# Performance work log

Measured on AMD Instinct MI355X. Metric: run time of the kernel, lower is better.

The kernel has to match this reference:

```python
import jax, jax.numpy as jnp
import numpy as np

EPS = 1e-5  # equinox LayerNorm default eps

def setup_inputs() -> dict:
    key = jax.random.key(0)
    k1, k2, k3, k4, k5 = jax.random.split(key, 5)
    heads, d, dH, N = 16, 1024, 64, 2048
    # lecun-normal-ish scaling for fan_in=d
    s = 1.0 / np.sqrt(d)
    return {
        "x": jax.random.normal(k1, (d, N), dtype=jnp.float32),
        "WQ": jax.random.normal(k2, (heads, d, dH), dtype=jnp.float32) * s,
        "WK": jax.random.normal(k3, (heads, d, dH), dtype=jnp.float32) * s,
        "WV": jax.random.normal(k4, (heads, d, dH), dtype=jnp.float32) * s,
        "W0": jax.random.normal(k5, (d, d), dtype=jnp.float32) * s,
    }

def reference(x, WQ, WK, WV, W0):
    # x: [d, N]
    residual = x
    # equinox LayerNorm over full shape (d, N), no affine params
    mean = jnp.mean(x)
    var = jnp.var(x)
    xn = (x - mean) * jax.lax.rsqrt(var + EPS)
    # project: [h, d_model, dH] x [d_model, N] -> [h, dH, N]
    Q = jnp.einsum('hcd,ci->hdi', WQ, xn)
    K = jnp.einsum('hcd,ci->hdi', WK, xn)
    V = jnp.einsum('hcd,ci->hdi', WV, xn)
    dH = WK.shape[-1]
    dot = jnp.einsum('hdi,hdj->hij', Q, K)  # [h, N, N]
    alpha = jax.nn.softmax(dot / jnp.sqrt(jnp.asarray(dH, dot.dtype)), axis=-1)
    attn = jnp.einsum('hij,hdj->hdi', alpha, V)  # [h, dH, N]
    N = attn.shape[2]
    attn = attn.reshape(-1, N)  # [d, N]
    out = W0 @ attn
    return out + residual
```

## Files before the change

### kernel.cpp

```cpp
#include <hip/hip_runtime.h>
#include <math.h>

typedef unsigned short u16;
typedef _Float16 f16;
typedef __attribute__((ext_vector_type(8))) short bf16x8;
typedef __attribute__((ext_vector_type(4))) float f32x4;
typedef __attribute__((ext_vector_type(4))) f16 f16x4;

#define D_MODEL 1024
#define SEQ_N   2048
#define HEADS   16
#define DHEAD   64
#define M3      3072
#define JSPLIT  2
#define JCHUNK  (SEQ_N / JSPLIT)
#define NIT     (JCHUNK / 64)
#define QSCALE  0.18033688011112042f
#define EXPOFF  5.770780163555854f

#define GLOBAL_AS __attribute__((address_space(1)))
#define LDS_AS    __attribute__((address_space(3)))
#define ASYNC16(gp, lp) __builtin_amdgcn_global_load_lds( \
    (const GLOBAL_AS unsigned int*)(gp), (LDS_AS unsigned int*)(lp), 16, 0, 0)

__device__ __forceinline__ u16 f2bf(float f) {
  union { float f; unsigned int u; } v; v.f = f;
  unsigned int r = v.u + 0x7fffu + ((v.u >> 16) & 1u);
  return (u16)(r >> 16);
}

__global__ __launch_bounds__(256) void prep(const float* __restrict__ x,
                                            double* __restrict__ part,
                                            const float* __restrict__ WQ,
                                            const float* __restrict__ WK,
                                            const float* __restrict__ WV,
                                            const float* __restrict__ W0,
                                            u16* __restrict__ Wp,
                                            u16* __restrict__ W0p) {
  __shared__ double ls[256], lss[256];
  __shared__ float tile[32][65];
  int t = threadIdx.x;
  int b = blockIdx.x;
  if (b < 256) {
    const float4* x4 = (const float4*)x;
    const int n4 = (D_MODEL * SEQ_N) / 4;
    double s = 0.0, ss = 0.0;
    for (int idx = b * 256 + t; idx < n4; idx += 256 * 256) {
      float4 v = x4[idx];
      s  += (double)v.x + (double)v.y + (double)v.z + (double)v.w;
      ss += (double)v.x * v.x + (double)v.y * v.y + (double)v.z * v.z + (double)v.w * v.w;
    }
    ls[t] = s; lss[t] = ss;
    __syncthreads();
    for (int off = 128; off > 0; off >>= 1) {
      if (t < off) { ls[t] += ls[t + off]; lss[t] += lss[t + off]; }
      __syncthreads();
    }
    if (t == 0) { part[2 * b] = ls[0]; part[2 * b + 1] = lss[0]; }
    return;
  }
  int f = b - 256;
  int z = f >> 9;
  int rem = f & 511;
  if (z == 3) {
    int idx = rem * 512 + t;
#pragma unroll
    for (int r = 0; r < 2; ++r, idx += 256) {
      float4 v = ((const float4*)W0)[idx];
      unsigned int lo = (unsigned int)f2bf(v.x) | ((unsigned int)f2bf(v.y) << 16);
      unsigned int hi = (unsigned int)f2bf(v.z) | ((unsigned int)f2bf(v.w) << 16);
      uint2 o; o.x = lo; o.y = hi;
      *(uint2*)(&W0p[(size_t)idx * 4]) = o;
    }
    return;
  }
  const float* W = (z == 0) ? WQ : ((z == 1) ? WK : WV);
  int h = rem >> 5, cb = (rem & 31) * 32;
  int dh = t & 63, cl = t >> 6;
  for (int r = 0; r < 8; ++r) {
    int c = cl + r * 4;
    tile[c][dh] = W[((size_t)h * D_MODEL + cb + c) * DHEAD + dh];
  }
  __syncthreads();
  int c2 = t & 31, d2 = t >> 5;
  for (int r = 0; r < 8; ++r) {
    int dd = d2 + r * 8;
    Wp[(size_t)((z * HEADS + h) * DHEAD + dd) * D_MODEL + cb + c2] = f2bf(tile[c2][dd]);
  }
}

__global__ __launch_bounds__(256) void ln_norm_t(const float* __restrict__ x,
                                                 const double* __restrict__ part,
                                                 u16* __restrict__ xnt) {
  __shared__ double ls[256], lss[256];
  __shared__ float tile[64][65];
  int t = threadIdx.x;
  ls[t] = part[2 * t]; lss[t] = part[2 * t + 1];
  __syncthreads();
  for (int off = 128; off > 0; off >>= 1) {
    if (t < off) { ls[t] += ls[t + off]; lss[t] += lss[t + off]; }
    __syncthreads();
  }
  double inv = 1.0 / ((double)D_MODEL * (double)SEQ_N);
  double m = ls[0] * inv;
  double vv = lss[0] * inv - m * m;
  float mean = (float)m;
  float rstd = (float)(1.0 / sqrt(vv + 1e-5));

  int ib = blockIdx.x * 64, cb = blockIdx.y * 64;
  int il = t & 63, cl = t >> 6;
  for (int r = 0; r < 16; ++r) {
    int c = cl + r * 4;
    tile[c][il] = (x[(size_t)(cb + c) * SEQ_N + ib + il] - mean) * rstd;
  }
  __syncthreads();
  int c2 = t & 63, i2 = t >> 6;
  for (int r = 0; r < 16; ++r) {
    int i = i2 + r * 4;
    xnt[(size_t)(ib + i) * D_MODEL + cb + c2] = f2bf(tile[c2][i]);
  }
}

__global__ __launch_bounds__(256) void gemm_qkv(const u16* __restrict__ A,
                                                const u16* __restrict__ Bt,
                                                u16* __restrict__ Qt,
                                                u16* __restrict__ Kt,
                                                f16* __restrict__ Vb) {
  __shared__ __align__(16) u16 Alds[2 * 2 * 96 * 32];
  __shared__ __align__(16) u16 Blds[2 * 2 * 128 * 32];
  int t = threadIdx.x;
  int lane = t & 63, w = t >> 6;
  int g = lane >> 4, l16 = lane & 15;
  int wr = w >> 1, wc = w & 1;
  int flat = blockIdx.x;
  int wi = flat >> 3;
  int wx = wi & 7, wy = wi >> 3;
  int cx = (flat & 7) & 1, cy = (flat & 7) >> 1;
  int bx = cx * 8 + wx;
  int by = cy * 8 + wy;
  int mb = by * 96, nb = bx * 128;

  f32x4 acc[3][4];
#pragma unroll
  for (int i = 0; i < 3; ++i)
#pragma unroll
    for (int j = 0; j < 4; ++j) acc[i][j] = (f32x4){0.f, 0.f, 0.f, 0.f};

  const u16* AgP[3]; int ldsA[3];
#pragma unroll
  for (int r = 0; r < 3; ++r) {
    int idx = r * 256 + t;
    int kk = (idx >= 384) ? 1 : 0;
    int rem = idx - kk * 384;
    int row = rem >> 2, c4 = rem & 3;
    int csw = c4 ^ ((row >> 1) & 3);
    AgP[r] = A + (size_t)(mb + row) * D_MODEL + kk * 32 + csw * 8;
    ldsA[r] = idx * 8;
  }
  const u16* BgP[4]; int ldsB[4];
#pragma unroll
  for (int r = 0; r < 4; ++r) {
    int idx = r * 256 + t;
    int kk = idx >> 9;
    int rem = idx & 511;
    int row = rem >> 2, c4 = rem & 3;
    int csw = c4 ^ ((row >> 1) & 3);
    BgP[r] = Bt + (size_t)(nb + row) * D_MODEL + kk * 32 + csw * 8;
    ldsB[r] = idx * 8;
  }

#pragma unroll
  for (int r = 0; r < 3; ++r) ASYNC16(AgP[r], &Alds[ldsA[r]]);
#pragma unroll
  for (int r = 0; r < 4; ++r) ASYNC16(BgP[r], &Blds[ldsB[r]]);
#pragma unroll
  for (int r = 0; r < 3; ++r) ASYNC16(AgP[r] + 64, &Alds[6144 + ldsA[r]]);
#pragma unroll
  for (int r = 0; r < 4; ++r) ASYNC16(BgP[r] + 64, &Blds[8192 + ldsB[r]]);

  int rowa0 = wr * 48, rowb0 = wc * 64;
  int cur = 0;
  for (int ks = 0; ks < 16; ++ks) {
    if (ks < 15) asm volatile("s_waitcnt vmcnt(7)" ::: "memory");
    else         asm volatile("s_waitcnt vmcnt(0)" ::: "memory");
    __builtin_amdgcn_s_barrier();
#pragma unroll
    for (int kk = 0; kk < 2; ++kk) {
      bf16x8 af[3], bf[4];
#pragma unroll
      for (int tm = 0; tm < 3; ++tm) {
        int row = rowa0 + tm * 16 + l16;
        int gs = g ^ ((row >> 1) & 3);
        af[tm] = *(const bf16x8*)(&Alds[cur * 6144 + kk * 3072 + row * 32 + gs * 8]);
      }
#pragma unroll
      for (int tn = 0; tn < 4; ++tn) {
        int row = rowb0 + tn * 16 + l16;
        int gs = g ^ ((row >> 1) & 3);
        bf[tn] = *(const bf16x8*)(&Blds[cur * 8192 + kk * 4096 + row * 32 + gs * 8]);
      }
#pragma unroll
      for (int tm = 0; tm < 3; ++tm)
#pragma unroll
        for (int tn = 0; tn < 4; ++tn)
          acc[tm][tn] = __builtin_amdgcn_mfma_f32_16x16x32_bf16(af[tm], bf[tn],
                                                                acc[tm][tn], 0, 0, 0);
    }
    __builtin_amdgcn_s_barrier();
    if (ks + 2 < 16) {
      int kb = (ks + 2) * 64;
#pragma unroll
      for (int r = 0; r < 3; ++r) ASYNC16(AgP[r] + kb, &Alds[cur * 6144 + ldsA[r]]);
#pragma unroll
      for (int r = 0; r < 4; ++r) ASYNC16(BgP[r] + kb, &Blds[cur * 8192 + ldsB[r]]);
    }
    cur ^= 1;
  }

#pragma unroll
  for (int tm = 0; tm < 3; ++tm) {
    int row0 = mb + wr * 48 + tm * 16 + g * 4;
#pragma unroll
    for (int tn = 0; tn < 4; ++tn) {
      int col = nb + wc * 64 + tn * 16 + l16;
      if (row0 < 2 * D_MODEL) {
        u16* T = (row0 < D_MODEL) ? Qt : Kt;
        float sc = (row0 < D_MODEL) ? QSCALE : 1.0f;
        int rbase = (row0 < D_MODEL) ? row0 : row0 - D_MODEL;
        ushort4 o;
        o.x = f2bf(acc[tm][tn][0] * sc); o.y = f2bf(acc[tm][tn][1] * sc);
        o.z = f2bf(acc[tm][tn][2] * sc); o.w = f2bf(acc[tm][tn][3] * sc);
        *(ushort4*)(&T[(size_t)col * D_MODEL + rbase]) = o;
      } else {
        int rbase = row0 - 2 * D_MODEL;
#pragma unroll
        for (int r = 0; r < 4; ++r)
          Vb[(size_t)(rbase + r) * SEQ_N + col] = (f16)acc[tm][tn][r];
      }
    }
  }
}

__global__ __launch_bounds__(256) void gemm_bf16(const u16* __restrict__ A,
                                                 const u16* __restrict__ Bt,
                                                 float* __restrict__ C,
                                                 const float* __restrict__ res,
                                                 int M, int N, int K) {
  __shared__ __align__(16) u16 Alds[2 * 2 * 64 * 32];
  __shared__ __align__(16) u16 Blds[2 * 2 * 64 * 32];
  int t = threadIdx.x;
  int w = t >> 6, lane = t & 63;
  int g = lane >> 4, l16 = lane & 15;
  int flat = blockIdx.x;
  int wi = flat >> 3;
  int wx = wi & 7, wy = wi >> 3;
  int cx = (flat & 7) & 3, cy = (flat & 7) >> 2;
  int bx = cx * 8 + wx;
  int by = cy * 8 + wy;
  int mb = by * 64, nb = bx * 64;
  f32x4 acc[4];
  for (int i = 0; i < 4; ++i) acc[i] = (f32x4){0.f, 0.f, 0.f, 0.f};

  const u16* AgP[2]; const u16* BgP[2]; int ldsO[2];
#pragma unroll
  for (int r = 0; r < 2; ++r) {
    int idx = r * 256 + t;
    int kk = idx >> 8;
    int rem = idx & 255;
    int row = rem >> 2, c4 = rem & 3;
    int csw = c4 ^ ((row >> 1) & 3);
    AgP[r] = A + (size_t)(mb + row) * K + kk * 32 + csw * 8;
    BgP[r] = Bt + (size_t)(nb + row) * K + kk * 32 + csw * 8;
    ldsO[r] = idx * 8;
  }

#pragma unroll
  for (int r = 0; r < 2; ++r) { ASYNC16(AgP[r], &Alds[ldsO[r]]); ASYNC16(BgP[r], &Blds[ldsO[r]]); }
#pragma unroll
  for (int r = 0; r < 2; ++r) {
    ASYNC16(AgP[r] + 64, &Alds[4096 + ldsO[r]]);
    ASYNC16(BgP[r] + 64, &Blds[4096 + ldsO[r]]);
  }

  int cur = 0;
  const int NK = 16;
  for (int ks = 0; ks < NK; ++ks) {
    if (ks < NK - 1) asm volatile("s_waitcnt vmcnt(4)" ::: "memory");
    else             asm volatile("s_waitcnt vmcnt(0)" ::: "memory");
    __builtin_amdgcn_s_barrier();
#pragma unroll
    for (int kk = 0; kk < 2; ++kk) {
      int rowa = w * 16 + l16;
      int gsa = g ^ ((rowa >> 1) & 3);
      bf16x8 af = *(const bf16x8*)(&Alds[cur * 4096 + kk * 2048 + rowa * 32 + gsa * 8]);
#pragma unroll
      for (int tn = 0; tn < 4; ++tn) {
        int rowb = tn * 16 + l16;
        int gsb = g ^ ((rowb >> 1) & 3);
        bf16x8 bf = *(const bf16x8*)(&Blds[cur * 4096 + kk * 2048 + rowb * 32 + gsb * 8]);
        acc[tn] = __builtin_amdgcn_mfma_f32_16x16x32_bf16(af, bf, acc[tn], 0, 0, 0);
      }
    }
    __builtin_amdgcn_s_barrier();
    if (ks + 2 < NK) {
      int kb = (ks + 2) * 64;
#pragma unroll
      for (int r = 0; r < 2; ++r) {
        ASYNC16(AgP[r] + kb, &Alds[cur * 4096 + ldsO[r]]);
        ASYNC16(BgP[r] + kb, &Blds[cur * 4096 + ldsO[r]]);
      }
    }
    cur ^= 1;
  }
  int col0 = nb + l16;
  int row0 = mb + w * 16 + g * 4;
#pragma unroll
  for (int tn = 0; tn < 4; ++tn) {
    int col = col0 + tn * 16;
#pragma unroll
    for (int r = 0; r < 4; ++r) {
      int row = row0 + r;
      float v = acc[tn][r];
      if (res) v += res[(size_t)row * N + col];
      C[(size_t)row * N + col] = v;
    }
  }
}

#define KSW(buf_, row_, ch_) ((buf_)*4096 + (row_)*64 + ((((ch_) ^ ((row_)&7)))*8))
__global__ __launch_bounds__(256, 2) void attn_mfma(const u16* __restrict__ Qt,
                                                    const u16* __restrict__ Kt,
                                                    const f16* __restrict__ Vb,
                                                    f16* __restrict__ Opart,
                                                    float* __restrict__ Lpart) {
  __shared__ __align__(16) u16 Klds[2 * 64 * 64];
  __shared__ __align__(16) f16 Vlds[2 * 64 * 64];
  int flat = blockIdx.x;
  int xcd = flat & 7, idx = flat >> 3;
  int h  = xcd * 2 + ((idx >> 5) & 1);
  int sp = idx >> 6;
  int ib = (idx & 31) * 64;
  int j0 = sp * JCHUNK;
  int t = threadIdx.x;
  int w = t >> 6, lane = t & 63;
  int g = lane >> 4, l16 = lane & 15;

  bf16x8 bq[2];
  {
    const u16* qb = Qt + (size_t)(ib + w * 16 + l16) * D_MODEL + h * DHEAD + g * 8;
    bq[0] = *(const bf16x8*)(qb);
    bq[1] = *(const bf16x8*)(qb + 32);
  }

  f32x4 acc_o[4];
#pragma unroll
  for (int i = 0; i < 4; ++i) acc_o[i] = (f32x4){0.f, 0.f, 0.f, 0.f};
  f32x4 acc_l = (f32x4){0.f, 0.f, 0.f, 0.f};
  f16x4 ones;
  ones[0] = (f16)1.f; ones[1] = (f16)1.f; ones[2] = (f16)1.f; ones[3] = (f16)1.f;

  const u16* KgP[2]; const f16* VgP[2]; int ldsS[2];
#pragma unroll
  for (int r = 0; r < 2; ++r) {
    int s = r * 256 + t;
    int row = s >> 3, pch = s & 7;
    int lch = pch ^ (row & 7);
    KgP[r] = Kt + (size_t)(j0 + row) * D_MODEL + h * DHEAD + lch * 8;
    VgP[r] = Vb + (size_t)(h * DHEAD + row) * SEQ_N + j0 + lch * 8;
    ldsS[r] = s * 8;
  }

#pragma unroll
  for (int r = 0; r < 2; ++r) { ASYNC16(KgP[r], &Klds[ldsS[r]]); ASYNC16(VgP[r], &Vlds[ldsS[r]]); }
#pragma unroll
  for (int r = 0; r < 2; ++r) {
    ASYNC16(KgP[r] + 64 * D_MODEL, &Klds[4096 + ldsS[r]]);
    ASYNC16(VgP[r] + 64,           &Vlds[4096 + ldsS[r]]);
  }

  int cur = 0;
  for (int it = 0; it < NIT; ++it) {
    if (it < NIT - 1) asm volatile("s_waitcnt vmcnt(4)" ::: "memory");
    else              asm volatile("s_waitcnt vmcnt(0)" ::: "memory");
    __builtin_amdgcn_s_barrier();

    f32x4 s[4];
#pragma unroll
    for (int i = 0; i < 4; ++i) s[i] = (f32x4){0.f, 0.f, 0.f, 0.f};
    __builtin_amdgcn_s_setprio(1);
#pragma unroll
    for (int kk = 0; kk < 2; ++kk)
#pragma unroll
      for (int tn = 0; tn < 4; ++tn) {
        int row = tn * 16 + l16;
        bf16x8 ak = *(const bf16x8*)(&Klds[KSW(cur, row, kk * 4 + g)]);
        s[tn] = __builtin_amdgcn_mfma_f32_16x16x32_bf16(ak, bq[kk], s[tn], 0, 0, 0);
      }
    __builtin_amdgcn_s_setprio(0);
    f16x4 pf[4];
#pragma unroll
    for (int tn = 0; tn < 4; ++tn) {
      f16x4 p;
#pragma unroll
      for (int r = 0; r < 4; ++r)
        p[r] = (f16)exp2f(s[tn][r] - EXPOFF);
      pf[tn] = p;
    }
    __builtin_amdgcn_s_setprio(1);
#pragma unroll
    for (int tn = 0; tn < 4; ++tn) {
      acc_l = __builtin_amdgcn_mfma_f32_16x16x16f16(pf[tn], ones, acc_l, 0, 0, 0);
#pragma unroll
      for (int td = 0; td < 4; ++td) {
        int row = td * 16 + l16;
        f16x4 bv = *(const f16x4*)(&Vlds[KSW(cur, row, tn * 2 + (g >> 1)) + (g & 1) * 4]);
        acc_o[td] =
            __builtin_amdgcn_mfma_f32_16x16x16f16(pf[tn], bv, acc_o[td], 0, 0, 0);
      }
    }
    __builtin_amdgcn_s_setprio(0);

    __builtin_amdgcn_s_barrier();
    if (it + 2 < NIT) {
      int joff = (it + 2) * 64;
#pragma unroll
      for (int r = 0; r < 2; ++r) {
        ASYNC16(KgP[r] + (size_t)joff * D_MODEL, &Klds[cur * 4096 + ldsS[r]]);
        ASYNC16(VgP[r] + joff,                   &Vlds[cur * 4096 + ldsS[r]]);
      }
    }
    cur ^= 1;
  }

  if (l16 == 0) {
#pragma unroll
    for (int r = 0; r < 4; ++r)
      Lpart[((size_t)sp * HEADS + h) * SEQ_N + ib + w * 16 + g * 4 + r] = acc_l[r];
  }

#pragma unroll
  for (int td = 0; td < 4; ++td) {
    int dh = h * DHEAD + td * 16 + l16;
#pragma unroll
    for (int r = 0; r < 4; ++r) {
      int i = ib + w * 16 + g * 4 + r;
      Opart[((size_t)sp * SEQ_N + i) * D_MODEL + dh] = (f16)acc_o[td][r];
    }
  }
}

__global__ __launch_bounds__(256) void attn_combine(const f16* __restrict__ Opart,
                                                    const float* __restrict__ Lpart,
                                                    u16* __restrict__ attnt) {
  int i = blockIdx.x;
  int c = threadIdx.x * 4;
  int h = c >> 6;
  float l = 0.f;
#pragma unroll
  for (int s = 0; s < JSPLIT; ++s) l += Lpart[((size_t)s * HEADS + h) * SEQ_N + i];
  float o[4] = {0.f, 0.f, 0.f, 0.f};
#pragma unroll
  for (int s = 0; s < JSPLIT; ++s) {
    f16x4 v = *(const f16x4*)(&Opart[((size_t)s * SEQ_N + i) * D_MODEL + c]);
#pragma unroll
    for (int r = 0; r < 4; ++r) o[r] += (float)v[r];
  }
  float inv = 1.0f / l;
  ushort4 ob;
  ob.x = f2bf(o[0] * inv); ob.y = f2bf(o[1] * inv);
  ob.z = f2bf(o[2] * inv); ob.w = f2bf(o[3] * inv);
  *(ushort4*)(&attnt[(size_t)i * D_MODEL + c]) = ob;
}

extern "C" void kernel_launch(void* const* d_in, const int* in_sizes, int n_in,
                              void* d_out, int out_size, void* d_ws, size_t ws_size,
                              hipStream_t stream) {
  const float* x  = (const float*)d_in[0];
  const float* WQ = (const float*)d_in[1];
  const float* WK = (const float*)d_in[2];
  const float* WV = (const float*)d_in[3];
  const float* W0 = (const float*)d_in[4];
  float* out = (float*)d_out;

  char* ws = (char*)d_ws;
  size_t off = 0;
  double* part  = (double*)(ws + off); off += 8192;
  u16*    xnt   = (u16*)(ws + off); off += (size_t)SEQ_N * D_MODEL * 2;
  u16*    Wp    = (u16*)(ws + off); off += (size_t)M3 * D_MODEL * 2;
  u16*    W0p   = (u16*)(ws + off); off += (size_t)D_MODEL * D_MODEL * 2;
  u16*    Qt    = (u16*)(ws + off); off += (size_t)SEQ_N * D_MODEL * 2;
  u16*    Kt    = (u16*)(ws + off); off += (size_t)SEQ_N * D_MODEL * 2;
  f16*    Vb    = (f16*)(ws + off); off += (size_t)D_MODEL * SEQ_N * 2;
  u16*    attnt = (u16*)(ws + off); off += (size_t)SEQ_N * D_MODEL * 2;
  f16*    Opart = (f16*)(ws + off); off += (size_t)JSPLIT * SEQ_N * D_MODEL * 2;
  float*  Lpart = (float*)(ws + off); off += (size_t)JSPLIT * HEADS * SEQ_N * 4;

  prep<<<256 + 2048, 256, 0, stream>>>(x, part, WQ, WK, WV, W0, Wp, W0p);
  ln_norm_t<<<dim3(SEQ_N / 64, D_MODEL / 64), 256, 0, stream>>>(x, part, xnt);
  gemm_qkv<<<512, 256, 0, stream>>>(Wp, xnt, Qt, Kt, Vb);
  attn_mfma<<<1024, 256, 0, stream>>>(Qt, Kt, Vb, Opart, Lpart);
  attn_combine<<<SEQ_N, 256, 0, stream>>>(Opart, Lpart, attnt);
  gemm_bf16<<<512, 256, 0, stream>>>(W0p, attnt, out, x, D_MODEL, SEQ_N, D_MODEL);
}
```

Before: 151.5 us.

## Double query rows per attention block to reuse K/V tiles across two M-subtiles

```diff
diff --git a/kernel.cpp b/kernel.cpp
--- a/kernel.cpp
+++ b/kernel.cpp
@@ -337,25 +337,30 @@
   __shared__ __align__(16) f16 Vlds[2 * 64 * 64];
   int flat = blockIdx.x;
   int xcd = flat & 7, idx = flat >> 3;
-  int h  = xcd * 2 + ((idx >> 5) & 1);
-  int sp = idx >> 6;
-  int ib = (idx & 31) * 64;
+  int h  = xcd * 2 + ((idx >> 4) & 1);
+  int sp = idx >> 5;
+  int ib = (idx & 15) * 128;
   int j0 = sp * JCHUNK;
   int t = threadIdx.x;
   int w = t >> 6, lane = t & 63;
   int g = lane >> 4, l16 = lane & 15;
 
-  bf16x8 bq[2];
-  {
-    const u16* qb = Qt + (size_t)(ib + w * 16 + l16) * D_MODEL + h * DHEAD + g * 8;
-    bq[0] = *(const bf16x8*)(qb);
-    bq[1] = *(const bf16x8*)(qb + 32);
-  }
-
-  f32x4 acc_o[4];
-#pragma unroll
-  for (int i = 0; i < 4; ++i) acc_o[i] = (f32x4){0.f, 0.f, 0.f, 0.f};
-  f32x4 acc_l = (f32x4){0.f, 0.f, 0.f, 0.f};
+  bf16x8 bq[2][2];
+#pragma unroll
+  for (int tm = 0; tm < 2; ++tm) {
+    const u16* qb = Qt + (size_t)(ib + w * 32 + tm * 16 + l16) * D_MODEL + h * DHEAD + g * 8;
+    bq[tm][0] = *(const bf16x8*)(qb);
+    bq[tm][1] = *(const bf16x8*)(qb + 32);
+  }
+
+  f32x4 acc_o[2][4];
+#pragma unroll
+  for (int tm = 0; tm < 2; ++tm)
+#pragma unroll
+    for (int i = 0; i < 4; ++i) acc_o[tm][i] = (f32x4){0.f, 0.f, 0.f, 0.f};
+  f32x4 acc_l[2];
+  acc_l[0] = (f32x4){0.f, 0.f, 0.f, 0.f};
+  acc_l[1] = (f32x4){0.f, 0.f, 0.f, 0.f};
   f16x4 ones;
   ones[0] = (f16)1.f; ones[1] = (f16)1.f; ones[2] = (f16)1.f; ones[3] = (f16)1.f;
 
@@ -384,9 +389,11 @@
     else              asm volatile("s_waitcnt vmcnt(0)" ::: "memory");
     __builtin_amdgcn_s_barrier();
 
-    f32x4 s[4];
-#pragma unroll
-    for (int i = 0; i < 4; ++i) s[i] = (f32x4){0.f, 0.f, 0.f, 0.f};
+    f32x4 s[2][4];
+#pragma unroll
+    for (int tm = 0; tm < 2; ++tm)
+#pragma unroll
+      for (int i = 0; i < 4; ++i) s[tm][i] = (f32x4){0.f, 0.f, 0.f, 0.f};
     __builtin_amdgcn_s_setprio(1);
 #pragma unroll
     for (int kk = 0; kk < 2; ++kk)
@@ -394,28 +401,36 @@
       for (int tn = 0; tn < 4; ++tn) {
         int row = tn * 16 + l16;
         bf16x8 ak = *(const bf16x8*)(&Klds[KSW(cur, row, kk * 4 + g)]);
-        s[tn] = __builtin_amdgcn_mfma_f32_16x16x32_bf16(ak, bq[kk], s[tn], 0, 0, 0);
+#pragma unroll
+        for (int tm = 0; tm < 2; ++tm)
+          s[tm][tn] = __builtin_amdgcn_mfma_f32_16x16x32_bf16(ak, bq[tm][kk],
+                                                              s[tm][tn], 0, 0, 0);
       }
     __builtin_amdgcn_s_setprio(0);
-    f16x4 pf[4];
+    f16x4 pf[2][4];
+#pragma unroll
+    for (int tm = 0; tm < 2; ++tm)
+#pragma unroll
+      for (int tn = 0; tn < 4; ++tn) {
+        f16x4 p;
+#pragma unroll
+        for (int r = 0; r < 4; ++r)
+          p[r] = (f16)exp2f(s[tm][tn][r] - EXPOFF);
+        pf[tm][tn] = p;
+      }
+    __builtin_amdgcn_s_setprio(1);
 #pragma unroll
     for (int tn = 0; tn < 4; ++tn) {
-      f16x4 p;
-#pragma unroll
-      for (int r = 0; r < 4; ++r)
-        p[r] = (f16)exp2f(s[tn][r] - EXPOFF);
-      pf[tn] = p;
-    }
-    __builtin_amdgcn_s_setprio(1);
-#pragma unroll
-    for (int tn = 0; tn < 4; ++tn) {
-      acc_l = __builtin_amdgcn_mfma_f32_16x16x16f16(pf[tn], ones, acc_l, 0, 0, 0);
+      acc_l[0] = __builtin_amdgcn_mfma_f32_16x16x16f16(pf[0][tn], ones, acc_l[0], 0, 0, 0);
+      acc_l[1] = __builtin_amdgcn_mfma_f32_16x16x16f16(pf[1][tn], ones, acc_l[1], 0, 0, 0);
 #pragma unroll
       for (int td = 0; td < 4; ++td) {
         int row = td * 16 + l16;
         f16x4 bv = *(const f16x4*)(&Vlds[KSW(cur, row, tn * 2 + (g >> 1)) + (g & 1) * 4]);
-        acc_o[td] =
-            __builtin_amdgcn_mfma_f32_16x16x16f16(pf[tn], bv, acc_o[td], 0, 0, 0);
+#pragma unroll
+        for (int tm = 0; tm < 2; ++tm)
+          acc_o[tm][td] =
+              __builtin_amdgcn_mfma_f32_16x16x16f16(pf[tm][tn], bv, acc_o[tm][td], 0, 0, 0);
       }
     }
     __builtin_amdgcn_s_setprio(0);
@@ -434,19 +449,24 @@
 
   if (l16 == 0) {
 #pragma unroll
-    for (int r = 0; r < 4; ++r)
-      Lpart[((size_t)sp * HEADS + h) * SEQ_N + ib + w * 16 + g * 4 + r] = acc_l[r];
-  }
-
-#pragma unroll
-  for (int td = 0; td < 4; ++td) {
-    int dh = h * DHEAD + td * 16 + l16;
-#pragma unroll
-    for (int r = 0; r < 4; ++r) {
-      int i = ib + w * 16 + g * 4 + r;
-      Opart[((size_t)sp * SEQ_N + i) * D_MODEL + dh] = (f16)acc_o[td][r];
-    }
-  }
+    for (int tm = 0; tm < 2; ++tm)
+#pragma unroll
+      for (int r = 0; r < 4; ++r)
+        Lpart[((size_t)sp * HEADS + h) * SEQ_N + ib + w * 32 + tm * 16 + g * 4 + r] =
+            acc_l[tm][r];
+  }
+
+#pragma unroll
+  for (int tm = 0; tm < 2; ++tm)
+#pragma unroll
+    for (int td = 0; td < 4; ++td) {
+      int dh = h * DHEAD + td * 16 + l16;
+#pragma unroll
+      for (int r = 0; r < 4; ++r) {
+        int i = ib + w * 32 + tm * 16 + g * 4 + r;
+        Opart[((size_t)sp * SEQ_N + i) * D_MODEL + dh] = (f16)acc_o[tm][td][r];
+      }
+    }
 }
 
 __global__ __launch_bounds__(256) void attn_combine(const f16* __restrict__ Opart,
@@ -498,7 +518,7 @@
   prep<<<256 + 2048, 256, 0, stream>>>(x, part, WQ, WK, WV, W0, Wp, W0p);
   ln_norm_t<<<dim3(SEQ_N / 64, D_MODEL / 64), 256, 0, stream>>>(x, part, xnt);
   gemm_qkv<<<512, 256, 0, stream>>>(Wp, xnt, Qt, Kt, Vb);
-  attn_mfma<<<1024, 256, 0, stream>>>(Qt, Kt, Vb, Opart, Lpart);
+  attn_mfma<<<512, 256, 0, stream>>>(Qt, Kt, Vb, Opart, Lpart);
   attn_combine<<<SEQ_N, 256, 0, stream>>>(Opart, Lpart, attnt);
   gemm_bf16<<<512, 256, 0, stream>>>(W0p, attnt, out, x, D_MODEL, SEQ_N, D_MODEL);
 }
```

New measurement: 155.8 us. +2.9%, slower.
